# Optimization experiments

Hardware: AMD Instinct MI355X
Metric: run time of the kernel (lower is better)

The kernel has to match this reference:

```python
import jax, jax.numpy as jnp
import numpy as np

N = 50000   # nodes
E = 1000000 # edges
D_IN = 64
D_OUT = 64
R = 16      # relations (num_rels == num_bases)


def setup_inputs() -> dict:
    key = jax.random.key(0)
    k1, k2, k3, k4, k5, k6, k7 = jax.random.split(key, 7)
    node_features = jax.random.normal(k1, (N, D_IN), dtype=jnp.float32)
    edge_src = jax.random.randint(k2, (E,), 0, N, dtype=jnp.int32)
    edge_dst = jax.random.randint(k3, (E,), 0, N, dtype=jnp.int32)
    edge_type = jax.random.randint(k4, (E,), 0, R, dtype=jnp.int32)
    edge_norm = jax.random.uniform(k5, (E,), dtype=jnp.float32)
    weight = jax.random.normal(k6, (R, D_IN, D_OUT), dtype=jnp.float32) * 0.1
    bias = jax.random.normal(k7, (D_OUT,), dtype=jnp.float32) * 0.1
    return {
        "node_features": node_features,
        "edge_src": edge_src,
        "edge_dst": edge_dst,
        "edge_type": edge_type,
        "edge_norm": edge_norm,
        "weight": weight,
        "bias": bias,
    }


def reference(node_features, edge_src, edge_dst, edge_type, edge_norm, weight, bias):
    # gather source features and per-edge relation weight matrices
    h_src = node_features[edge_src]              # [E, D_IN]
    w = weight[edge_type]                        # [E, D_IN, D_OUT]
    # per-edge bmm: [E,1,D_IN] @ [E,D_IN,D_OUT] -> [E,D_OUT]
    msg = jnp.einsum('ed,edo->eo', h_src, w)
    msg = msg * edge_norm[:, None]               # norm scaling
    # scatter-sum aggregation over destination nodes
    node_repr = jax.ops.segment_sum(msg, edge_dst, num_segments=N)  # [N, D_OUT]
    node_repr = node_repr + bias
    return jax.nn.relu(node_repr)
```

## Files before the change

### kernel.cpp

```cpp
#include <hip/hip_runtime.h>
#include <hip/hip_bf16.h>


#define NN 50000
#define EE 1000000
#define RR 16
#define NBLK 256
#define EPB 3907
#define BSH 6
#define NBUK 782
#define NS (NBUK * NBLK)
#define SCAP 2048

typedef __attribute__((ext_vector_type(8))) short short8;
typedef __attribute__((ext_vector_type(4))) float f32x4;

static __device__ inline unsigned short f2bf(float f) {
  union { __hip_bfloat16 h; unsigned short u; } cv;
  cv.h = __float2bfloat16(f);
  return cv.u;
}
static __device__ inline float bf2f(unsigned short u) {
  union { unsigned i; float f; } cv;
  cv.i = ((unsigned)u) << 16;
  return cv.f;
}

__global__ __launch_bounds__(256) void k_wt(const float* __restrict__ W,
                                            unsigned short* __restrict__ Wt) {
  __shared__ __align__(16) unsigned short Wl[64][72];
  const int r = blockIdx.x, tid = threadIdx.x;
  for (int i = tid; i < 4096; i += 256) Wl[i & 63][i >> 6] = f2bf(W[(r << 12) + i]);
  __syncthreads();
  const int o = tid >> 2, kc = (tid & 3) << 4;
  const short8 v0 = *reinterpret_cast<const short8*>(&Wl[o][kc]);
  const short8 v1 = *reinterpret_cast<const short8*>(&Wl[o][kc + 8]);
  unsigned short* dst = Wt + (r << 12) + (o << 6) + kc;
  *reinterpret_cast<short8*>(dst) = v0;
  *reinterpret_cast<short8*>(dst + 8) = v1;
}

__global__ __launch_bounds__(512) void k_gemm(const float* __restrict__ nf,
                                              const unsigned short* __restrict__ Wt,
                                              unsigned short* __restrict__ X) {
  __shared__ __align__(16) unsigned short Wl[4][64][72];
  const int tid = threadIdx.x;
  const int lane = tid & 63, wv = tid >> 6;
  const int lr = lane & 15, lg = lane >> 4;
  const int node = (blockIdx.x << 7) + (wv << 4) + lr;
  const int r0 = blockIdx.y << 2;
  #pragma unroll
  for (int rr = 0; rr < 4; ++rr) {
    const short8 v = *reinterpret_cast<const short8*>(
        Wt + (((size_t)(r0 + rr)) << 12) + (tid << 3));
    *reinterpret_cast<short8*>(&Wl[rr][tid >> 3][(tid & 7) << 3]) = v;
  }
  short8 bf0, bf1;
  if (node < NN) {
    const float* ap = nf + (size_t)node * 64 + lg * 8;
    float4 v0 = *reinterpret_cast<const float4*>(ap);
    float4 v1 = *reinterpret_cast<const float4*>(ap + 4);
    float4 v2 = *reinterpret_cast<const float4*>(ap + 32);
    float4 v3 = *reinterpret_cast<const float4*>(ap + 36);
    bf0 = short8{(short)f2bf(v0.x), (short)f2bf(v0.y), (short)f2bf(v0.z), (short)f2bf(v0.w),
                 (short)f2bf(v1.x), (short)f2bf(v1.y), (short)f2bf(v1.z), (short)f2bf(v1.w)};
    bf1 = short8{(short)f2bf(v2.x), (short)f2bf(v2.y), (short)f2bf(v2.z), (short)f2bf(v2.w),
                 (short)f2bf(v3.x), (short)f2bf(v3.y), (short)f2bf(v3.z), (short)f2bf(v3.w)};
  } else {
    bf0 = short8{0, 0, 0, 0, 0, 0, 0, 0};
    bf1 = bf0;
  }
  __syncthreads();
  #pragma unroll
  for (int rr = 0; rr < 4; ++rr) {
    const int r = r0 + rr;
    short8 a[8];
    #pragma unroll
    for (int c = 0; c < 4; ++c) {
      a[2 * c] = *reinterpret_cast<const short8*>(&Wl[rr][(c << 4) + lr][lg << 3]);
      a[2 * c + 1] = *reinterpret_cast<const short8*>(&Wl[rr][(c << 4) + lr][32 + (lg << 3)]);
    }
    f32x4 acc[4];
    #pragma unroll
    for (int c = 0; c < 4; ++c) {
      acc[c] = f32x4{0.f, 0.f, 0.f, 0.f};
      acc[c] = __builtin_amdgcn_mfma_f32_16x16x32_bf16(a[2 * c], bf0, acc[c], 0, 0, 0);
      acc[c] = __builtin_amdgcn_mfma_f32_16x16x32_bf16(a[2 * c + 1], bf1, acc[c], 0, 0, 0);
    }
    if (node < NN) {
      #pragma unroll
      for (int c = 0; c < 4; ++c) {
        uint2 p;
        p.x = (unsigned)f2bf(acc[c][0]) | ((unsigned)f2bf(acc[c][1]) << 16);
        p.y = (unsigned)f2bf(acc[c][2]) | ((unsigned)f2bf(acc[c][3]) << 16);
        *reinterpret_cast<uint2*>(&X[((size_t)r * NN + node) * 64 + (c << 4) + (lg << 2)]) = p;
      }
    }
  }
}

__global__ __launch_bounds__(256) void k_hist(const int* __restrict__ edst,
                                              int* __restrict__ cntT) {
  __shared__ int cnt[NBUK];
  const int bl = blockIdx.x, tid = threadIdx.x;
  for (int i = tid; i < NBUK; i += 256) cnt[i] = 0;
  __syncthreads();
  const int e0 = bl * EPB, e1 = min(EE, e0 + EPB);
  for (int e = e0 + tid; e < e1; e += 256) atomicAdd(&cnt[edst[e] >> BSH], 1);
  __syncthreads();
  for (int i = tid; i < NBUK; i += 256) cntT[i * NBLK + bl] = cnt[i];
}

__global__ __launch_bounds__(256) void k_scan_a(const int* __restrict__ cntT,
                                                int* __restrict__ offsT,
                                                int* __restrict__ bsum) {
  __shared__ int s[256];
  const int t = threadIdx.x;
  const int i = blockIdx.x * 256 + t;
  const int v = cntT[i];
  s[t] = v;
  __syncthreads();
  #pragma unroll
  for (int off = 1; off < 256; off <<= 1) {
    const int x = (t >= off) ? s[t - off] : 0;
    __syncthreads();
    s[t] += x;
    __syncthreads();
  }
  offsT[i] = s[t] - v;
  if (t == 255) bsum[blockIdx.x] = s[255];
}

__global__ __launch_bounds__(1024) void k_scan_b(int* __restrict__ bsum) {
  __shared__ int s[1024];
  const int t = threadIdx.x;
  const int v = (t < NBUK) ? bsum[t] : 0;
  s[t] = v;
  __syncthreads();
  #pragma unroll
  for (int off = 1; off < 1024; off <<= 1) {
    const int x = (t >= off) ? s[t - off] : 0;
    __syncthreads();
    s[t] += x;
    __syncthreads();
  }
  if (t < NBUK) bsum[t] = s[t] - v;
}

__global__ __launch_bounds__(256) void k_scan_c(int* __restrict__ offsT,
                                                const int* __restrict__ bsum) {
  const int i = blockIdx.x * 256 + threadIdx.x;
  offsT[i] += bsum[blockIdx.x];
}

__global__ __launch_bounds__(256) void k_scatter(const int* __restrict__ esrc,
                                                 const int* __restrict__ edst,
                                                 const int* __restrict__ etyp,
                                                 const float* __restrict__ enorm,
                                                 const int* __restrict__ offsT,
                                                 uint2* __restrict__ rec) {
  __shared__ int cur[NBUK];
  const int bl = blockIdx.x, tid = threadIdx.x;
  for (int i = tid; i < NBUK; i += 256) cur[i] = offsT[i * NBLK + bl];
  __syncthreads();
  const int e0 = bl * EPB, e1 = min(EE, e0 + EPB);
  for (int e = e0 + tid; e < e1; e += 256) {
    const int d = edst[e];
    const int pos = atomicAdd(&cur[d >> BSH], 1);
    rec[pos] = make_uint2(((unsigned)(etyp[e] * NN + esrc[e]) << 6) | (unsigned)(d & 63),
                          __float_as_uint(enorm[e]));
  }
}

__global__ __launch_bounds__(256) void k_nsort(const int* __restrict__ offsT,
                                               uint2* __restrict__ rec,
                                               int* __restrict__ noffs) {
  __shared__ uint2 sbuf[SCAP];
  __shared__ int cnt[64], cur[64];
  const int bu = blockIdx.x, tid = threadIdx.x;
  const int s = offsT[bu * NBLK];
  const int e = (bu == NBUK - 1) ? EE : offsT[(bu + 1) * NBLK];
  const int n = e - s;
  if (tid < 64) cnt[tid] = 0;
  __syncthreads();
  if (n > SCAP) {
    if (tid < 64) noffs[(bu << BSH) + tid] = -1;
    return;
  }
  for (int i = tid; i < n; i += 256) {
    const uint2 r = rec[s + i];
    sbuf[i] = r;
    atomicAdd(&cnt[r.x & 63u], 1);
  }
  __syncthreads();
  if (tid < 64) {
    const int v = cnt[tid];
    int x = v;
    #pragma unroll
    for (int off = 1; off < 64; off <<= 1) {
      const int t = __shfl_up(x, off, 64);
      if (tid >= off) x += t;
    }
    cur[tid] = x - v;
    noffs[(bu << BSH) + tid] = s + x - v;
  }
  __syncthreads();
  for (int i = tid; i < n; i += 256) {
    const uint2 r = sbuf[i];
    const int pos = atomicAdd(&cur[r.x & 63u], 1);
    rec[s + pos] = r;
  }
}

__global__ __launch_bounds__(256) void k_ngather(const uint2* __restrict__ rec,
                                                 const int* __restrict__ noffs,
                                                 const int* __restrict__ offsT,
                                                 const unsigned short* __restrict__ X,
                                                 const float* __restrict__ bias,
                                                 float* __restrict__ out) {
  const int w = (int)((blockIdx.x * 256 + threadIdx.x) >> 6);
  const int lane = threadIdx.x & 63;
  if (w >= NN) return;
  const int quarter = lane >> 4, d4 = lane & 15;
  const int bu = w >> BSH;
  float4 acc = {0.f, 0.f, 0.f, 0.f};
  const int jb = noffs[w];
  if (jb >= 0) {
    const int bend = (bu == NBUK - 1) ? EE : offsT[(bu + 1) * NBLK];
    const int je = ((w & 63) == 63) ? bend : noffs[w + 1];
    for (int base = jb; base < je; base += 64) {
      const int deg = min(64, je - base);
      unsigned rxs = 0;
      float rns = 0.f;
      if (lane < deg) {
        const uint2 r = rec[base + lane];
        rxs = r.x >> 6;
        rns = __uint_as_float(r.y);
      }
      int u = 0;
      for (; u + 8 <= deg; u += 8) {
        const int i0 = u + quarter, i1 = u + 4 + quarter;
        const unsigned row0 = (unsigned)__shfl((int)rxs, i0, 64);
        const float n0 = __shfl(rns, i0, 64);
        const unsigned row1 = (unsigned)__shfl((int)rxs, i1, 64);
        const float n1 = __shfl(rns, i1, 64);
        const uint2 x0 = *reinterpret_cast<const uint2*>(X + (size_t)row0 * 64 + (d4 << 2));
        const uint2 x1 = *reinterpret_cast<const uint2*>(X + (size_t)row1 * 64 + (d4 << 2));
        acc.x = fmaf(n0, bf2f((unsigned short)(x0.x & 0xffffu)), acc.x);
        acc.y = fmaf(n0, bf2f((unsigned short)(x0.x >> 16)), acc.y);
        acc.z = fmaf(n0, bf2f((unsigned short)(x0.y & 0xffffu)), acc.z);
        acc.w = fmaf(n0, bf2f((unsigned short)(x0.y >> 16)), acc.w);
        acc.x = fmaf(n1, bf2f((unsigned short)(x1.x & 0xffffu)), acc.x);
        acc.y = fmaf(n1, bf2f((unsigned short)(x1.x >> 16)), acc.y);
        acc.z = fmaf(n1, bf2f((unsigned short)(x1.y & 0xffffu)), acc.z);
        acc.w = fmaf(n1, bf2f((unsigned short)(x1.y >> 16)), acc.w);
      }
      for (; u < deg; u += 4) {
        const int i = u + quarter;
        const int ic = min(i, deg - 1);
        const unsigned row = (unsigned)__shfl((int)rxs, ic, 64);
        float n = __shfl(rns, ic, 64);
        n = (i < deg) ? n : 0.f;
        const uint2 x = *reinterpret_cast<const uint2*>(X + (size_t)row * 64 + (d4 << 2));
        acc.x = fmaf(n, bf2f((unsigned short)(x.x & 0xffffu)), acc.x);
        acc.y = fmaf(n, bf2f((unsigned short)(x.x >> 16)), acc.y);
        acc.z = fmaf(n, bf2f((unsigned short)(x.y & 0xffffu)), acc.z);
        acc.w = fmaf(n, bf2f((unsigned short)(x.y >> 16)), acc.w);
      }
    }
  } else {
    if (quarter == 0) {
      const int s = offsT[bu * NBLK];
      const int e = (bu == NBUK - 1) ? EE : offsT[(bu + 1) * NBLK];
      const unsigned dl = (unsigned)(w & 63);
      for (int j = s; j < e; ++j) {
        const uint2 r = rec[j];
        if ((r.x & 63u) == dl) {
          const float n = __uint_as_float(r.y);
          const uint2 x =
              *reinterpret_cast<const uint2*>(X + (size_t)(r.x >> 6) * 64 + (d4 << 2));
          acc.x = fmaf(n, bf2f((unsigned short)(x.x & 0xffffu)), acc.x);
          acc.y = fmaf(n, bf2f((unsigned short)(x.x >> 16)), acc.y);
          acc.z = fmaf(n, bf2f((unsigned short)(x.y & 0xffffu)), acc.z);
          acc.w = fmaf(n, bf2f((unsigned short)(x.y >> 16)), acc.w);
        }
      }
    }
  }
  acc.x += __shfl_xor(acc.x, 16, 64);
  acc.y += __shfl_xor(acc.y, 16, 64);
  acc.z += __shfl_xor(acc.z, 16, 64);
  acc.w += __shfl_xor(acc.w, 16, 64);
  acc.x += __shfl_xor(acc.x, 32, 64);
  acc.y += __shfl_xor(acc.y, 32, 64);
  acc.z += __shfl_xor(acc.z, 32, 64);
  acc.w += __shfl_xor(acc.w, 32, 64);
  if (quarter == 0) {
    const float4 b = reinterpret_cast<const float4*>(bias)[d4];
    float4 o;
    o.x = fmaxf(acc.x + b.x, 0.f);
    o.y = fmaxf(acc.y + b.y, 0.f);
    o.z = fmaxf(acc.z + b.z, 0.f);
    o.w = fmaxf(acc.w + b.w, 0.f);
    reinterpret_cast<float4*>(out)[(size_t)w * 16 + d4] = o;
  }
}

extern "C" void kernel_launch(void* const* d_in, const int* in_sizes, int n_in,
                              void* d_out, int out_size, void* d_ws, size_t ws_size,
                              hipStream_t stream) {
  const float* nf = (const float*)d_in[0];
  const int* esrc = (const int*)d_in[1];
  const int* edst = (const int*)d_in[2];
  const int* etyp = (const int*)d_in[3];
  const float* enorm = (const float*)d_in[4];
  const float* W = (const float*)d_in[5];
  const float* bias = (const float*)d_in[6];
  float* out = (float*)d_out;

  char* ws = (char*)d_ws;
  unsigned short* X = (unsigned short*)ws;
  unsigned short* Wt = (unsigned short*)(ws + 102400000);
  uint2* rec = (uint2*)(ws + 102531072);
  int* cntT = (int*)(ws + 110531072);
  int* offsT = (int*)(ws + 111331840);
  int* bsum = (int*)(ws + 112132608);
  int* noffs = (int*)(ws + 112135736);

  k_wt<<<RR, 256, 0, stream>>>(W, Wt);
  dim3 g1((NN + 127) / 128, 4);
  k_gemm<<<g1, 512, 0, stream>>>(nf, Wt, X);

  k_hist<<<NBLK, 256, 0, stream>>>(edst, cntT);
  k_scan_a<<<NS / 256, 256, 0, stream>>>(cntT, offsT, bsum);
  k_scan_b<<<1, 1024, 0, stream>>>(bsum);
  k_scan_c<<<NS / 256, 256, 0, stream>>>(offsT, bsum);
  k_scatter<<<NBLK, 256, 0, stream>>>(esrc, edst, etyp, enorm, offsT, rec);
  k_nsort<<<NBUK, 256, 0, stream>>>(offsT, rec, noffs);

  k_ngather<<<(NN * 64 + 255) / 256, 256, 0, stream>>>(rec, noffs, offsT, X, bias, out);
}
```

Measured before the change: 117.0 us.

## Fuse weight transpose, GEMM and histogram into one launch; drop scan fixup kernel

Merges the weight-transpose, per-relation GEMM and destination histogram into a single heterogeneous kernel. The first blocks compute the histogram and the rest convert weights to bf16 in shared memory and run the MFMA GEMM. The scan-add kernel is removed: the bucket base offsets are kept in a separate array (with a sentinel at the end) and added where they are consumed, in scatter, nsort and gather. This cuts launch count and per-launch overhead, but every GEMM block now re-transposes 4 relation weight matrices from fp32, and the GEMM uses 256-thread blocks over 64 nodes instead of 512-thread blocks over 128 nodes.

```diff
diff --git a/kernel.cpp b/kernel.cpp
--- a/kernel.cpp
+++ b/kernel.cpp
@@ -26,34 +26,32 @@
   return cv.f;
 }
 
-__global__ __launch_bounds__(256) void k_wt(const float* __restrict__ W,
-                                            unsigned short* __restrict__ Wt) {
-  __shared__ __align__(16) unsigned short Wl[64][72];
-  const int r = blockIdx.x, tid = threadIdx.x;
-  for (int i = tid; i < 4096; i += 256) Wl[i & 63][i >> 6] = f2bf(W[(r << 12) + i]);
-  __syncthreads();
-  const int o = tid >> 2, kc = (tid & 3) << 4;
-  const short8 v0 = *reinterpret_cast<const short8*>(&Wl[o][kc]);
-  const short8 v1 = *reinterpret_cast<const short8*>(&Wl[o][kc + 8]);
-  unsigned short* dst = Wt + (r << 12) + (o << 6) + kc;
-  *reinterpret_cast<short8*>(dst) = v0;
-  *reinterpret_cast<short8*>(dst + 8) = v1;
-}
-
-__global__ __launch_bounds__(512) void k_gemm(const float* __restrict__ nf,
-                                              const unsigned short* __restrict__ Wt,
-                                              unsigned short* __restrict__ X) {
-  __shared__ __align__(16) unsigned short Wl[4][64][72];
-  const int tid = threadIdx.x;
+__global__ __launch_bounds__(256) void k_gemm_hist(const float* __restrict__ nf,
+                                                   const float* __restrict__ W,
+                                                   const int* __restrict__ edst,
+                                                   unsigned short* __restrict__ X,
+                                                   int* __restrict__ cntT) {
+  __shared__ __align__(16) char smem[4 * 64 * 72 * 2];
+  const int bid = blockIdx.x, tid = threadIdx.x;
+  if (bid < NBLK) {
+    int* cnt = reinterpret_cast<int*>(smem);
+    for (int i = tid; i < NBUK; i += 256) cnt[i] = 0;
+    __syncthreads();
+    const int e0 = bid * EPB, e1 = min(EE, e0 + EPB);
+    for (int e = e0 + tid; e < e1; e += 256) atomicAdd(&cnt[edst[e] >> BSH], 1);
+    __syncthreads();
+    for (int i = tid; i < NBUK; i += 256) cntT[i * NBLK + bid] = cnt[i];
+    return;
+  }
+  auto Wl = reinterpret_cast<unsigned short(*)[64][72]>(smem);
+  const int g = bid - NBLK;
+  const int bx = g >> 2, r0 = (g & 3) << 2;
   const int lane = tid & 63, wv = tid >> 6;
   const int lr = lane & 15, lg = lane >> 4;
-  const int node = (blockIdx.x << 7) + (wv << 4) + lr;
-  const int r0 = blockIdx.y << 2;
-  #pragma unroll
-  for (int rr = 0; rr < 4; ++rr) {
-    const short8 v = *reinterpret_cast<const short8*>(
-        Wt + (((size_t)(r0 + rr)) << 12) + (tid << 3));
-    *reinterpret_cast<short8*>(&Wl[rr][tid >> 3][(tid & 7) << 3]) = v;
+  const int node = (bx << 6) + (wv << 4) + lr;
+  for (int i = tid; i < 16384; i += 256) {
+    const int rr = i >> 12, rem = i & 4095;
+    Wl[rr][rem & 63][rem >> 6] = f2bf(W[(((size_t)(r0 + rr)) << 12) + rem]);
   }
   short8 bf0, bf1;
   if (node < NN) {
@@ -99,18 +97,6 @@
   }
 }
 
-__global__ __launch_bounds__(256) void k_hist(const int* __restrict__ edst,
-                                              int* __restrict__ cntT) {
-  __shared__ int cnt[NBUK];
-  const int bl = blockIdx.x, tid = threadIdx.x;
-  for (int i = tid; i < NBUK; i += 256) cnt[i] = 0;
-  __syncthreads();
-  const int e0 = bl * EPB, e1 = min(EE, e0 + EPB);
-  for (int e = e0 + tid; e < e1; e += 256) atomicAdd(&cnt[edst[e] >> BSH], 1);
-  __syncthreads();
-  for (int i = tid; i < NBUK; i += 256) cntT[i * NBLK + bl] = cnt[i];
-}
-
 __global__ __launch_bounds__(256) void k_scan_a(const int* __restrict__ cntT,
                                                 int* __restrict__ offsT,
                                                 int* __restrict__ bsum) {
@@ -131,7 +117,8 @@
   if (t == 255) bsum[blockIdx.x] = s[255];
 }
 
-__global__ __launch_bounds__(1024) void k_scan_b(int* __restrict__ bsum) {
+__global__ __launch_bounds__(1024) void k_scan_b(const int* __restrict__ bsum,
+                                                 int* __restrict__ bsum2) {
   __shared__ int s[1024];
   const int t = threadIdx.x;
   const int v = (t < NBUK) ? bsum[t] : 0;
@@ -144,13 +131,8 @@
     s[t] += x;
     __syncthreads();
   }
-  if (t < NBUK) bsum[t] = s[t] - v;
-}
-
-__global__ __launch_bounds__(256) void k_scan_c(int* __restrict__ offsT,
-                                                const int* __restrict__ bsum) {
-  const int i = blockIdx.x * 256 + threadIdx.x;
-  offsT[i] += bsum[blockIdx.x];
+  if (t < NBUK) bsum2[t] = s[t] - v;
+  if (t == NBUK) bsum2[NBUK] = EE;
 }
 
 __global__ __launch_bounds__(256) void k_scatter(const int* __restrict__ esrc,
@@ -158,10 +140,11 @@
                                                  const int* __restrict__ etyp,
                                                  const float* __restrict__ enorm,
                                                  const int* __restrict__ offsT,
+                                                 const int* __restrict__ bsum2,
                                                  uint2* __restrict__ rec) {
   __shared__ int cur[NBUK];
   const int bl = blockIdx.x, tid = threadIdx.x;
-  for (int i = tid; i < NBUK; i += 256) cur[i] = offsT[i * NBLK + bl];
+  for (int i = tid; i < NBUK; i += 256) cur[i] = offsT[i * NBLK + bl] + bsum2[i];
   __syncthreads();
   const int e0 = bl * EPB, e1 = min(EE, e0 + EPB);
   for (int e = e0 + tid; e < e1; e += 256) {
@@ -172,14 +155,14 @@
   }
 }
 
-__global__ __launch_bounds__(256) void k_nsort(const int* __restrict__ offsT,
+__global__ __launch_bounds__(256) void k_nsort(const int* __restrict__ bsum2,
                                                uint2* __restrict__ rec,
                                                int* __restrict__ noffs) {
   __shared__ uint2 sbuf[SCAP];
   __shared__ int cnt[64], cur[64];
   const int bu = blockIdx.x, tid = threadIdx.x;
-  const int s = offsT[bu * NBLK];
-  const int e = (bu == NBUK - 1) ? EE : offsT[(bu + 1) * NBLK];
+  const int s = bsum2[bu];
+  const int e = bsum2[bu + 1];
   const int n = e - s;
   if (tid < 64) cnt[tid] = 0;
   __syncthreads();
@@ -214,7 +197,7 @@
 
 __global__ __launch_bounds__(256) void k_ngather(const uint2* __restrict__ rec,
                                                  const int* __restrict__ noffs,
-                                                 const int* __restrict__ offsT,
+                                                 const int* __restrict__ bsum2,
                                                  const unsigned short* __restrict__ X,
                                                  const float* __restrict__ bias,
                                                  float* __restrict__ out) {
@@ -226,8 +209,7 @@
   float4 acc = {0.f, 0.f, 0.f, 0.f};
   const int jb = noffs[w];
   if (jb >= 0) {
-    const int bend = (bu == NBUK - 1) ? EE : offsT[(bu + 1) * NBLK];
-    const int je = ((w & 63) == 63) ? bend : noffs[w + 1];
+    const int je = ((w & 63) == 63) ? bsum2[bu + 1] : noffs[w + 1];
     for (int base = jb; base < je; base += 64) {
       const int deg = min(64, je - base);
       unsigned rxs = 0;
@@ -270,8 +252,8 @@
     }
   } else {
     if (quarter == 0) {
-      const int s = offsT[bu * NBLK];
-      const int e = (bu == NBUK - 1) ? EE : offsT[(bu + 1) * NBLK];
+      const int s = bsum2[bu];
+      const int e = bsum2[bu + 1];
       const unsigned dl = (unsigned)(w & 63);
       for (int j = s; j < e; ++j) {
         const uint2 r = rec[j];
@@ -320,23 +302,17 @@
 
   char* ws = (char*)d_ws;
   unsigned short* X = (unsigned short*)ws;
-  unsigned short* Wt = (unsigned short*)(ws + 102400000);
-  uint2* rec = (uint2*)(ws + 102531072);
-  int* cntT = (int*)(ws + 110531072);
-  int* offsT = (int*)(ws + 111331840);
-  int* bsum = (int*)(ws + 112132608);
-  int* noffs = (int*)(ws + 112135736);
-
-  k_wt<<<RR, 256, 0, stream>>>(W, Wt);
-  dim3 g1((NN + 127) / 128, 4);
-  k_gemm<<<g1, 512, 0, stream>>>(nf, Wt, X);
-
-  k_hist<<<NBLK, 256, 0, stream>>>(edst, cntT);
+  uint2* rec = (uint2*)(ws + 102400000);
+  int* cntT = (int*)(ws + 110400000);
+  int* offsT = (int*)(ws + 111200768);
+  int* bsum = (int*)(ws + 112001536);
+  int* bsum2 = (int*)(ws + 112004664);
+  int* noffs = (int*)(ws + 112007796);
+
+  k_gemm_hist<<<NBLK + NBUK * 4, 256, 0, stream>>>(nf, W, edst, X, cntT);
   k_scan_a<<<NS / 256, 256, 0, stream>>>(cntT, offsT, bsum);
-  k_scan_b<<<1, 1024, 0, stream>>>(bsum);
-  k_scan_c<<<NS / 256, 256, 0, stream>>>(offsT, bsum);
-  k_scatter<<<NBLK, 256, 0, stream>>>(esrc, edst, etyp, enorm, offsT, rec);
-  k_nsort<<<NBUK, 256, 0, stream>>>(offsT, rec, noffs);
-
-  k_ngather<<<(NN * 64 + 255) / 256, 256, 0, stream>>>(rec, noffs, offsT, X, bias, out);
-}
+  k_scan_b<<<1, 1024, 0, stream>>>(bsum, bsum2);
+  k_scatter<<<NBLK, 256, 0, stream>>>(esrc, edst, etyp, enorm, offsT, bsum2, rec);
+  k_nsort<<<NBUK, 256, 0, stream>>>(bsum2, rec, noffs);
+  k_ngather<<<(NN * 64 + 255) / 256, 256, 0, stream>>>(rec, noffs, bsum2, X, bias, out);
+}
```

New measurement: 109.5 us. 6.4% less time.
